# Performance work log

Measured on AMD Instinct MI355X. Metric: run time of the kernel, lower is better.

Reference implementation:

```python
import jax, jax.numpy as jnp
import numpy as np

N_NODES = 50000
N_EDGES = 800000
D_IN = 128
D_HID = 128
D_OUT = 128


def _glorot(key, shape):
    fan_in, fan_out = shape
    lim = np.sqrt(6.0 / (fan_in + fan_out))
    return jax.random.uniform(key, shape, jnp.float32, -lim, lim)


def setup_inputs() -> dict:
    key = jax.random.key(0)
    ks = jax.random.split(key, 8)
    x = jax.random.normal(ks[0], (N_NODES, D_IN), jnp.float32)
    edge_index = jax.random.randint(ks[1], (2, N_EDGES), 0, N_NODES, jnp.int64)
    # SAGEConv layer 1: lin_l (neighbor aggregate, has bias), lin_r (root, no bias)
    W1l = _glorot(ks[2], (D_IN, D_HID))
    b1 = jnp.zeros((D_HID,), jnp.float32)
    W1r = _glorot(ks[3], (D_IN, D_HID))
    # SAGEConv layer 2
    W2l = _glorot(ks[4], (D_HID, D_OUT))
    b2 = jnp.zeros((D_OUT,), jnp.float32)
    W2r = _glorot(ks[5], (D_HID, D_OUT))
    return {"x": x, "edge_index": edge_index, "W1l": W1l, "b1": b1,
            "W1r": W1r, "W2l": W2l, "b2": b2, "W2r": W2r}


def _sage_conv(x, src, dst, Wl, bl, Wr):
    # mean-aggregate neighbor features j -> i, then out = mean @ Wl + b + x @ Wr
    msg_sum = jax.ops.segment_sum(x[src], dst, num_segments=N_NODES)  # [N, F]
    cnt = jax.ops.segment_sum(jnp.ones((src.shape[0],), x.dtype), dst,
                              num_segments=N_NODES)  # [N]
    mean = msg_sum / jnp.maximum(cnt, 1.0)[:, None]
    return mean @ Wl + bl + x @ Wr


def reference(x, edge_index, W1l, b1, W1r, W2l, b2, W2r):
    src, dst = edge_index[0], edge_index[1]
    h = _sage_conv(x, src, dst, W1l, b1, W1r)
    h = jax.nn.relu(h)
    # dropout(p=0.2) is identity in eval mode
    out = _sage_conv(h, src, dst, W2l, b2, W2r)
    return out
```

## Files before the change

### kernel.cpp

```cpp
#include <hip/hip_runtime.h>

#define N_NODES 50000
#define N_EDGES 800000
#define D 128
#define CAP 64
#define NPB 512
#define NBIN 98
#define BIN_CAP 12288
#define EPB 4096

typedef __attribute__((ext_vector_type(8))) short s16x8;
typedef __attribute__((ext_vector_type(8))) unsigned short u16x8;
typedef __attribute__((ext_vector_type(4))) unsigned short u16x4;
typedef __attribute__((ext_vector_type(4))) float f32x4;

__device__ __forceinline__ unsigned short f2bf(float f) {
    unsigned u = __builtin_bit_cast(unsigned, f);
    return (unsigned short)((u + 0x7FFFu + ((u >> 16) & 1u)) >> 16);
}
__device__ __forceinline__ float bf2f(unsigned short h) {
    return __builtin_bit_cast(float, (unsigned)h << 16);
}

__device__ __forceinline__ int load_src(const int* ei, int is32, int e) {
    return is32 ? ei[e] : ei[2 * e];
}
__device__ __forceinline__ int load_dst(const int* ei, int is32, int e) {
    return is32 ? ei[N_EDGES + e] : ei[2 * N_EDGES + 2 * e];
}

__global__ void zbin_kernel(int* __restrict__ bin_cnt) {
    bin_cnt[threadIdx.x] = 0;
}

__global__ __launch_bounds__(256) void prepbin_kernel(
    const float* __restrict__ x, const int* __restrict__ ei,
    const float* __restrict__ W1l, const float* __restrict__ W1r,
    const float* __restrict__ W2l, const float* __restrict__ W2r,
    unsigned short* __restrict__ xb, unsigned short* __restrict__ wt1,
    unsigned short* __restrict__ wt2, int* __restrict__ bin_cnt,
    unsigned* __restrict__ bins) {
    __shared__ unsigned sBuf[EPB];
    __shared__ int bcnt[128], brun[128], bpos[128], gbase[128];
    __shared__ int sAny;
    int b = blockIdx.x;
    int tid = threadIdx.x;
    if (b < 3125) {
        int t = b * 256 + tid;
        float4 a = *(const float4*)(x + (size_t)t * 8);
        float4 c = *(const float4*)(x + (size_t)t * 8 + 4);
        u16x8 o;
        o[0] = f2bf(a.x); o[1] = f2bf(a.y); o[2] = f2bf(a.z); o[3] = f2bf(a.w);
        o[4] = f2bf(c.x); o[5] = f2bf(c.y); o[6] = f2bf(c.z); o[7] = f2bf(c.w);
        *(u16x8*)(xb + (size_t)t * 8) = o;
        return;
    }
    if (b < 3381) {
        int idx = b - 3125;
        int layer = idx >> 7;
        int c = idx & 127;
        const float* Wl = layer ? W2l : W1l;
        const float* Wr = layer ? W2r : W1r;
        unsigned short* wt = layer ? wt2 : wt1;
        float v = (tid < 128) ? Wl[(size_t)tid * 128 + c]
                              : Wr[(size_t)(tid - 128) * 128 + c];
        wt[c * 256 + tid] = f2bf(v);
        return;
    }
    int blk = b - 3381;
    int e0 = blk * EPB + tid * 16;
    int nblk = N_EDGES - blk * EPB;
    if (nblk > EPB) nblk = EPB;
    bool valid = (tid * 16) < nblk;
    if (tid == 0) sAny = 0;
    if (tid < 128) bcnt[tid] = 0;
    __syncthreads();
    if (ei[2 * tid + 1] != 0) atomicOr(&sAny, 1);
    __syncthreads();
    int is32 = sAny;
    unsigned packed[16];
    if (valid) {
        if (is32) {
            const int4* ps = (const int4*)(ei + e0);
            const int4* pd = (const int4*)(ei + N_EDGES + e0);
#pragma unroll
            for (int q = 0; q < 4; ++q) {
                int4 s = ps[q], d = pd[q];
                packed[q * 4 + 0] = ((unsigned)d.x << 16) | (unsigned)s.x;
                packed[q * 4 + 1] = ((unsigned)d.y << 16) | (unsigned)s.y;
                packed[q * 4 + 2] = ((unsigned)d.z << 16) | (unsigned)s.z;
                packed[q * 4 + 3] = ((unsigned)d.w << 16) | (unsigned)s.w;
            }
        } else {
            const int4* ps = (const int4*)(ei + 2 * (size_t)e0);
            const int4* pd = (const int4*)(ei + 2 * (size_t)N_EDGES + 2 * (size_t)e0);
#pragma unroll
            for (int q = 0; q < 8; ++q) {
                int4 s = ps[q], d = pd[q];
                packed[q * 2 + 0] = ((unsigned)d.x << 16) | (unsigned)s.x;
                packed[q * 2 + 1] = ((unsigned)d.z << 16) | (unsigned)s.z;
            }
        }
#pragma unroll
        for (int k = 0; k < 16; ++k) atomicAdd(&bcnt[packed[k] >> 25], 1);
    }
    __syncthreads();
    if (tid < 64) {
        int a = bcnt[2 * tid], bb = bcnt[2 * tid + 1];
        int s = a + bb;
        int incl = s;
#pragma unroll
        for (int o = 1; o < 64; o <<= 1) {
            int t = __shfl_up(incl, o, 64);
            if (tid >= o) incl += t;
        }
        int pref = incl - s;
        brun[2 * tid] = pref;
        brun[2 * tid + 1] = pref + a;
        bpos[2 * tid] = pref;
        bpos[2 * tid + 1] = pref + a;
    }
    __syncthreads();
    if (valid) {
#pragma unroll
        for (int k = 0; k < 16; ++k) {
            int bin = packed[k] >> 25;
            int slot = atomicAdd(&bpos[bin], 1);
            sBuf[slot] = packed[k];
        }
    }
    __syncthreads();
    if (tid < 128) {
        int n = bcnt[tid];
        gbase[tid] = n > 0 ? atomicAdd(&bin_cnt[tid], n) : 0;
    }
    __syncthreads();
    for (int i = tid; i < nblk; i += 256) {
        unsigned p = sBuf[i];
        int bin = p >> 25;
        int gpos = gbase[bin] + (i - brun[bin]);
        if (gpos < BIN_CAP) bins[(size_t)bin * BIN_CAP + gpos] = p;
    }
}

__global__ __launch_bounds__(256) void unbin_kernel(const int* __restrict__ bin_cnt,
                                                    const unsigned* __restrict__ bins,
                                                    int* __restrict__ cnt,
                                                    unsigned short* __restrict__ srcs16) {
    __shared__ unsigned short buck[NPB * CAP];
    __shared__ int lcnt[NPB];
    int tid = threadIdx.x;
    int bn = blockIdx.x;
    int nbase = bn * NPB;
    for (int i = tid; i < NPB; i += 256) lcnt[i] = 0;
    __syncthreads();
    int nE = bin_cnt[bn];
    if (nE > BIN_CAP) nE = BIN_CAP;
    for (int i = tid; i < nE; i += 256) {
        unsigned p = bins[(size_t)bn * BIN_CAP + i];
        int local = (int)(p >> 16) - nbase;
        if ((unsigned)local < NPB) {
            int slot = atomicAdd(&lcnt[local], 1);
            if (slot < CAP) buck[local * CAP + slot] = (unsigned short)(p & 0xFFFFu);
        }
    }
    __syncthreads();
    int nlim = N_NODES - nbase;
    if (nlim > NPB) nlim = NPB;
    const uint4* sb = (const uint4*)buck;
    uint4* go = (uint4*)(srcs16 + (size_t)nbase * CAP);
    int n4 = nlim * 8;
    for (int i = tid; i < n4; i += 256) go[i] = sb[i];
    for (int i = tid; i < nlim; i += 256) cnt[nbase + i] = lcnt[i];
}

__global__ __launch_bounds__(256) void aggp_kernel(const unsigned short* __restrict__ feat,
                                                   const int* __restrict__ cnt,
                                                   const unsigned short* __restrict__ srcs16,
                                                   unsigned short* __restrict__ agg) {
    int node = blockIdx.x * 4 + (threadIdx.x >> 6);
    if (node >= N_NODES) return;
    int lane = threadIdx.x & 63;
    int q = lane >> 4;
    int c16 = lane & 15;
    int deg = cnt[node];
    int idx = srcs16[(size_t)node * CAP + lane];
    int d = deg < CAP ? deg : CAP;
    float acc[8] = {};
    for (int j = 0; j < d; j += 16) {
        int e[4];
        float m[4];
#pragma unroll
        for (int u = 0; u < 4; ++u) {
            int jj = j + u * 4 + q;
            int es = __shfl(idx, jj, 64);
            bool val = jj < d;
            e[u] = val ? es : 0;
            m[u] = val ? 1.f : 0.f;
        }
        u16x8 v[4];
#pragma unroll
        for (int u = 0; u < 4; ++u)
            v[u] = *((const u16x8*)(feat + (size_t)e[u] * D) + c16);
#pragma unroll
        for (int u = 0; u < 4; ++u)
#pragma unroll
            for (int i = 0; i < 8; ++i)
                acc[i] += bf2f((unsigned short)v[u][i]) * m[u];
    }
#pragma unroll
    for (int i = 0; i < 8; ++i) {
        acc[i] += __shfl_xor(acc[i], 16, 64);
        acc[i] += __shfl_xor(acc[i], 32, 64);
    }
    if (q == 0) {
        float s = deg > 0 ? 1.f / (float)deg : 0.f;
        u16x8 o;
#pragma unroll
        for (int i = 0; i < 8; ++i) o[i] = f2bf(acc[i] * s);
        *((u16x8*)(agg + (size_t)node * D) + c16) = o;
    }
}

template <int MODE>
__global__ __launch_bounds__(256) void mm3_kernel(const unsigned short* __restrict__ Agb,
                                                  const unsigned short* __restrict__ Rootb,
                                                  const unsigned short* __restrict__ Wt,
                                                  const float* __restrict__ bias,
                                                  float* __restrict__ C,
                                                  unsigned short* __restrict__ Cb) {
    __shared__ __align__(16) unsigned short sA[2][32][128];
    int r0 = blockIdx.x * 32;
    int tid = threadIdx.x;
    int lane = tid & 63, wid = tid >> 6;
    int l15 = lane & 15, khalf = lane >> 4;

    s16x8 bF[2][4][2];
#pragma unroll
    for (int p = 0; p < 2; ++p)
#pragma unroll
        for (int kc2 = 0; kc2 < 4; ++kc2)
#pragma unroll
            for (int nf = 0; nf < 2; ++nf) {
                int cc = wid * 32 + nf * 16 + l15;
                bF[p][kc2][nf] = *(const s16x8*)(Wt + (size_t)cc * 256 + p * 128 +
                                                 kc2 * 32 + khalf * 8);
            }
    {
        int r = tid >> 3;
        int kq = tid & 7;
        int row = r0 + r;
        u16x8 a0, a1, x0, x1;
        if (row < N_NODES) {
            const u16x8* pa = (const u16x8*)(Agb + (size_t)row * D + kq * 16);
            a0 = pa[0]; a1 = pa[1];
            const u16x8* pr = (const u16x8*)(Rootb + (size_t)row * D + kq * 16);
            x0 = pr[0]; x1 = pr[1];
        } else {
            u16x8 z = {};
            a0 = z; a1 = z; x0 = z; x1 = z;
        }
        int c0 = (kq * 2) ^ (r & 7), c1 = (kq * 2 + 1) ^ (r & 7);
        *(u16x8*)&sA[0][r][c0 * 8] = a0;
        *(u16x8*)&sA[0][r][c1 * 8] = a1;
        *(u16x8*)&sA[1][r][c0 * 8] = x0;
        *(u16x8*)&sA[1][r][c1 * 8] = x1;
    }
    __syncthreads();

    f32x4 acc[2][2] = {};
#pragma unroll
    for (int p = 0; p < 2; ++p)
#pragma unroll
        for (int kc2 = 0; kc2 < 4; ++kc2) {
            s16x8 aF[2];
#pragma unroll
            for (int mf = 0; mf < 2; ++mf) {
                int rr = mf * 16 + l15;
                int chunk = (kc2 * 4 + khalf) ^ (rr & 7);
                aF[mf] = *(const s16x8*)&sA[p][rr][chunk * 8];
            }
#pragma unroll
            for (int nf = 0; nf < 2; ++nf)
#pragma unroll
                for (int mf = 0; mf < 2; ++mf)
                    acc[mf][nf] = __builtin_amdgcn_mfma_f32_16x16x32_bf16(
                        aF[mf], bF[p][kc2][nf], acc[mf][nf], 0, 0, 0);
        }

#pragma unroll
    for (int mf = 0; mf < 2; ++mf)
#pragma unroll
        for (int nf = 0; nf < 2; ++nf) {
            int col = wid * 32 + nf * 16 + l15;
            float b = bias[col];
#pragma unroll
            for (int r = 0; r < 4; ++r) {
                int row = r0 + mf * 16 + khalf * 4 + r;
                if (row < N_NODES) {
                    float o = acc[mf][nf][r] + b;
                    if (MODE == 1) {
                        o = fmaxf(o, 0.f);
                        Cb[(size_t)row * D + col] = f2bf(o);
                    } else {
                        C[(size_t)row * D + col] = o;
                    }
                }
            }
        }
}

__global__ void initc_kernel(const int* __restrict__ ei, int* __restrict__ flag,
                             int* __restrict__ cnt) {
    int i = blockIdx.x * 256 + threadIdx.x;
    if (i < 50048) cnt[i] = 0;
    if (blockIdx.x == 0) {
        __shared__ int any;
        if (threadIdx.x == 0) any = 0;
        __syncthreads();
        if (ei[2 * threadIdx.x + 1] != 0) atomicOr(&any, 1);
        __syncthreads();
        if (threadIdx.x == 0) flag[0] = any;
    }
}

__global__ void prep_wf_kernel(const float* __restrict__ W1l, const float* __restrict__ W1r,
                               const float* __restrict__ W2l, const float* __restrict__ W2r,
                               unsigned short* __restrict__ wt1,
                               unsigned short* __restrict__ wt2) {
    int layer = blockIdx.x >> 7;
    int c = blockIdx.x & 127;
    int k = threadIdx.x;
    const float* Wl = layer ? W2l : W1l;
    const float* Wr = layer ? W2r : W1r;
    unsigned short* wt = layer ? wt2 : wt1;
    float v = (k < 128) ? Wl[(size_t)k * 128 + c] : Wr[(size_t)(k - 128) * 128 + c];
    wt[c * 256 + k] = f2bf(v);
}

__global__ void tobf_kernel(const float* __restrict__ in, unsigned short* __restrict__ out,
                            int n8) {
    int t = blockIdx.x * 256 + threadIdx.x;
    if (t >= n8) return;
    float4 a = *(const float4*)(in + (size_t)t * 8);
    float4 b = *(const float4*)(in + (size_t)t * 8 + 4);
    u16x8 o;
    o[0] = f2bf(a.x); o[1] = f2bf(a.y); o[2] = f2bf(a.z); o[3] = f2bf(a.w);
    o[4] = f2bf(b.x); o[5] = f2bf(b.y); o[6] = f2bf(b.z); o[7] = f2bf(b.w);
    *(u16x8*)(out + (size_t)t * 8) = o;
}

__global__ void hist_kernel(const int* __restrict__ ei, const int* __restrict__ flag,
                            int* __restrict__ cnt) {
    int e = blockIdx.x * blockDim.x + threadIdx.x;
    if (e >= N_EDGES) return;
    int is32 = flag[0];
    atomicAdd(&cnt[load_dst(ei, is32, e)], 1);
}

__global__ __launch_bounds__(1024) void scan_kernel(int* __restrict__ cnt_cur,
                                                    int* __restrict__ off) {
    __shared__ int wsum[16];
    __shared__ int woff[16];
    __shared__ int carry;
    __shared__ int tile_tot;
    int lane = threadIdx.x & 63;
    int wid = threadIdx.x >> 6;
    if (threadIdx.x == 0) carry = 0;
    __syncthreads();
    for (int base = 0; base < N_NODES; base += 1024) {
        int i = base + threadIdx.x;
        int v = (i < N_NODES) ? cnt_cur[i] : 0;
        int incl = v;
#pragma unroll
        for (int o = 1; o < 64; o <<= 1) {
            int t = __shfl_up(incl, o, 64);
            if (lane >= o) incl += t;
        }
        if (lane == 63) wsum[wid] = incl;
        __syncthreads();
        if (wid == 0 && lane < 16) {
            int t = wsum[lane];
            int inc2 = t;
#pragma unroll
            for (int o = 1; o < 16; o <<= 1) {
                int u = __shfl_up(inc2, o, 64);
                if (lane >= o) inc2 += u;
            }
            woff[lane] = inc2 - t;
            if (lane == 15) tile_tot = inc2;
        }
        __syncthreads();
        int c = carry;
        if (i < N_NODES) {
            int o = c + woff[wid] + (incl - v);
            off[i] = o;
            cnt_cur[i] = o;
        }
        __syncthreads();
        if (threadIdx.x == 0) carry = c + tile_tot;
        __syncthreads();
    }
    if (threadIdx.x == 0) off[N_NODES] = carry;
}

__global__ void fillc_kernel(const int* __restrict__ ei, const int* __restrict__ flag,
                             int* __restrict__ cur, int* __restrict__ srcs) {
    int e = blockIdx.x * blockDim.x + threadIdx.x;
    if (e >= N_EDGES) return;
    int is32 = flag[0];
    int d = load_dst(ei, is32, e);
    int p = atomicAdd(&cur[d], 1);
    srcs[p] = load_src(ei, is32, e);
}

__global__ __launch_bounds__(256) void aggc_kernel(const unsigned short* __restrict__ feat,
                                                   const int* __restrict__ off,
                                                   const int* __restrict__ srcs,
                                                   unsigned short* __restrict__ agg) {
    int node = blockIdx.x * 4 + (threadIdx.x >> 6);
    if (node >= N_NODES) return;
    int lane = threadIdx.x & 63;
    int half = lane >> 5;
    int c8 = lane & 31;
    int s0 = off[node], s1 = off[node + 1];
    int deg = s1 - s0;
    float a0 = 0.f, a1 = 0.f, a2 = 0.f, a3 = 0.f;
    for (int j = s0; j < s1; j += 2) {
        int jj = j + half;
        if (jj < s1) {
            int e = srcs[jj];
            u16x4 v = *((const u16x4*)(feat + (size_t)e * D) + c8);
            a0 += bf2f((unsigned short)v[0]);
            a1 += bf2f((unsigned short)v[1]);
            a2 += bf2f((unsigned short)v[2]);
            a3 += bf2f((unsigned short)v[3]);
        }
    }
    a0 += __shfl_xor(a0, 32, 64);
    a1 += __shfl_xor(a1, 32, 64);
    a2 += __shfl_xor(a2, 32, 64);
    a3 += __shfl_xor(a3, 32, 64);
    if (half == 0) {
        float s = deg > 0 ? 1.f / (float)deg : 0.f;
        u16x4 o;
        o[0] = f2bf(a0 * s); o[1] = f2bf(a1 * s);
        o[2] = f2bf(a2 * s); o[3] = f2bf(a3 * s);
        *((u16x4*)(agg + (size_t)node * D) + c8) = o;
    }
}

extern "C" void kernel_launch(void* const* d_in, const int* in_sizes, int n_in,
                              void* d_out, int out_size, void* d_ws, size_t ws_size,
                              hipStream_t stream) {
    const float* x = (const float*)d_in[0];
    const int* ei = (const int*)d_in[1];
    const float* W1l = (const float*)d_in[2];
    const float* b1 = (const float*)d_in[3];
    const float* W1r = (const float*)d_in[4];
    const float* W2l = (const float*)d_in[5];
    const float* b2 = (const float*)d_in[6];
    const float* W2r = (const float*)d_in[7];
    float* out = (float*)d_out;

    const size_t padded_need = 512 + (size_t)NBIN * BIN_CAP * 4 +
                               (size_t)50176 * CAP * 2 + 50048 * 4 + 2 * 65536 +
                               2 * (size_t)N_NODES * D * 2;

    if (ws_size >= padded_need) {
        char* w = (char*)d_ws;
        int* bin_cnt = (int*)w;                   w += 512;
        unsigned* bins = (unsigned*)w;            w += (size_t)NBIN * BIN_CAP * 4;
        unsigned short* srcs16 = (unsigned short*)w; w += (size_t)50176 * CAP * 2;
        int* cnt = (int*)w;                       w += 50048 * 4;
        unsigned short* wt1 = (unsigned short*)w; w += 65536;
        unsigned short* wt2 = (unsigned short*)w; w += 65536;
        unsigned short* xb = (unsigned short*)w;  w += (size_t)N_NODES * D * 2;
        unsigned short* hb = (unsigned short*)w;

        zbin_kernel<<<1, 128, 0, stream>>>(bin_cnt);
        prepbin_kernel<<<3577, 256, 0, stream>>>(x, ei, W1l, W1r, W2l, W2r, xb, wt1,
                                                 wt2, bin_cnt, bins);
        unbin_kernel<<<NBIN, 256, 0, stream>>>(bin_cnt, bins, cnt, srcs16);

        int nblk = (N_NODES + 31) / 32;
        aggp_kernel<<<(N_NODES + 3) / 4, 256, 0, stream>>>(xb, cnt, srcs16, hb);
        mm3_kernel<1><<<nblk, 256, 0, stream>>>(hb, xb, wt1, b1, nullptr, xb);

        aggp_kernel<<<(N_NODES + 3) / 4, 256, 0, stream>>>(xb, cnt, srcs16, hb);
        mm3_kernel<2><<<nblk, 256, 0, stream>>>(hb, xb, wt2, b2, out, nullptr);
    } else {
        char* w = (char*)d_ws;
        int* flag = (int*)w;                      w += 256;
        int* cur = (int*)w;                       w += 50048 * 4;
        int* off = (int*)w;                       w += 50056 * 4;
        int* srcs = (int*)w;                      w += (size_t)N_EDGES * 4;
        unsigned short* wt1 = (unsigned short*)w; w += 65536;
        unsigned short* wt2 = (unsigned short*)w; w += 65536;
        unsigned short* xb = (unsigned short*)w;  w += (size_t)N_NODES * D * 2;
        unsigned short* aggb = (unsigned short*)w;

        initc_kernel<<<196, 256, 0, stream>>>(ei, flag, cur);
        prep_wf_kernel<<<256, 256, 0, stream>>>(W1l, W1r, W2l, W2r, wt1, wt2);
        tobf_kernel<<<(N_NODES * D / 8 + 255) / 256, 256, 0, stream>>>(x, xb, N_NODES * D / 8);
        hist_kernel<<<(N_EDGES + 255) / 256, 256, 0, stream>>>(ei, flag, cur);
        scan_kernel<<<1, 1024, 0, stream>>>(cur, off);
        fillc_kernel<<<(N_EDGES + 255) / 256, 256, 0, stream>>>(ei, flag, cur, srcs);

        int nblk = (N_NODES + 31) / 32;
        aggc_kernel<<<(N_NODES + 3) / 4, 256, 0, stream>>>(xb, off, srcs, aggb);
        mm3_kernel<1><<<nblk, 256, 0, stream>>>(aggb, xb, wt1, b1, nullptr, xb);

        aggc_kernel<<<(N_NODES + 3) / 4, 256, 0, stream>>>(xb, off, srcs, aggb);
        mm3_kernel<2><<<nblk, 256, 0, stream>>>(aggb, xb, wt2, b2, out, nullptr);
    }
}
```

Baseline: 131.8 us.

## Fuse neighbor mean aggregation with dual-matmul into one kernel per layer

Replaces the separate aggregation and matmul kernels with a single 1024-thread kernel per layer. Each of 16 waves aggregates one node into shared memory, then the waves split the two K-halves (aggregate and root) across MFMA and reduce the partial results through shared memory. This removes the global round trip of the aggregated bf16 buffer and two launches per forward pass. In exchange it uses a small 16-row tile with reloaded weight fragments per block and an extra LDS reduction stage. The layer-1 output now goes to a separate buffer instead of overwriting xb.

```diff
diff --git a/kernel.cpp b/kernel.cpp
--- a/kernel.cpp
+++ b/kernel.cpp
@@ -174,140 +174,101 @@
     for (int i = tid; i < nlim; i += 256) cnt[nbase + i] = lcnt[i];
 }
 
-__global__ __launch_bounds__(256) void aggp_kernel(const unsigned short* __restrict__ feat,
-                                                   const int* __restrict__ cnt,
-                                                   const unsigned short* __restrict__ srcs16,
-                                                   unsigned short* __restrict__ agg) {
-    int node = blockIdx.x * 4 + (threadIdx.x >> 6);
-    if (node >= N_NODES) return;
-    int lane = threadIdx.x & 63;
-    int q = lane >> 4;
-    int c16 = lane & 15;
-    int deg = cnt[node];
-    int idx = srcs16[(size_t)node * CAP + lane];
-    int d = deg < CAP ? deg : CAP;
-    float acc[8] = {};
-    for (int j = 0; j < d; j += 16) {
-        int e[4];
-        float m[4];
-#pragma unroll
-        for (int u = 0; u < 4; ++u) {
-            int jj = j + u * 4 + q;
-            int es = __shfl(idx, jj, 64);
-            bool val = jj < d;
-            e[u] = val ? es : 0;
-            m[u] = val ? 1.f : 0.f;
-        }
-        u16x8 v[4];
-#pragma unroll
-        for (int u = 0; u < 4; ++u)
-            v[u] = *((const u16x8*)(feat + (size_t)e[u] * D) + c16);
-#pragma unroll
-        for (int u = 0; u < 4; ++u)
-#pragma unroll
-            for (int i = 0; i < 8; ++i)
-                acc[i] += bf2f((unsigned short)v[u][i]) * m[u];
-    }
-#pragma unroll
-    for (int i = 0; i < 8; ++i) {
-        acc[i] += __shfl_xor(acc[i], 16, 64);
-        acc[i] += __shfl_xor(acc[i], 32, 64);
-    }
-    if (q == 0) {
-        float s = deg > 0 ? 1.f / (float)deg : 0.f;
-        u16x8 o;
-#pragma unroll
-        for (int i = 0; i < 8; ++i) o[i] = f2bf(acc[i] * s);
-        *((u16x8*)(agg + (size_t)node * D) + c16) = o;
-    }
-}
-
 template <int MODE>
-__global__ __launch_bounds__(256) void mm3_kernel(const unsigned short* __restrict__ Agb,
-                                                  const unsigned short* __restrict__ Rootb,
-                                                  const unsigned short* __restrict__ Wt,
-                                                  const float* __restrict__ bias,
-                                                  float* __restrict__ C,
-                                                  unsigned short* __restrict__ Cb) {
-    __shared__ __align__(16) unsigned short sA[2][32][128];
-    int r0 = blockIdx.x * 32;
+__global__ __launch_bounds__(1024, 4) void fused16_kernel(
+    const unsigned short* __restrict__ feat,
+    const int* __restrict__ cnt,
+    const unsigned short* __restrict__ srcs16,
+    const unsigned short* __restrict__ Wt,
+    const float* __restrict__ bias,
+    float* __restrict__ C, unsigned short* __restrict__ Cb) {
+    __shared__ __align__(16) unsigned short sA[2][16][128];
+    __shared__ __align__(16) float sP[8][64][4];
+    int r0 = blockIdx.x * 16;
     int tid = threadIdx.x;
     int lane = tid & 63, wid = tid >> 6;
     int l15 = lane & 15, khalf = lane >> 4;
-
-    s16x8 bF[2][4][2];
-#pragma unroll
-    for (int p = 0; p < 2; ++p)
-#pragma unroll
-        for (int kc2 = 0; kc2 < 4; ++kc2)
-#pragma unroll
-            for (int nf = 0; nf < 2; ++nf) {
-                int cc = wid * 32 + nf * 16 + l15;
-                bF[p][kc2][nf] = *(const s16x8*)(Wt + (size_t)cc * 256 + p * 128 +
-                                                 kc2 * 32 + khalf * 8);
-            }
+    int p = wid >> 3, cf = wid & 7;
+
+    s16x8 bF[4];
+#pragma unroll
+    for (int kc2 = 0; kc2 < 4; ++kc2)
+        bF[kc2] = *(const s16x8*)(Wt + (size_t)(cf * 16 + l15) * 256 + p * 128 +
+                                  kc2 * 32 + khalf * 8);
+
+    if (tid < 256) {
+        int r = tid >> 4, ck = tid & 15;
+        u16x8 v = *(const u16x8*)(feat + (size_t)(r0 + r) * D + ck * 8);
+        *(u16x8*)&sA[1][r][(ck ^ (r & 7)) * 8] = v;
+    }
+
     {
-        int r = tid >> 3;
-        int kq = tid & 7;
-        int row = r0 + r;
-        u16x8 a0, a1, x0, x1;
-        if (row < N_NODES) {
-            const u16x8* pa = (const u16x8*)(Agb + (size_t)row * D + kq * 16);
-            a0 = pa[0]; a1 = pa[1];
-            const u16x8* pr = (const u16x8*)(Rootb + (size_t)row * D + kq * 16);
-            x0 = pr[0]; x1 = pr[1];
-        } else {
-            u16x8 z = {};
-            a0 = z; a1 = z; x0 = z; x1 = z;
-        }
-        int c0 = (kq * 2) ^ (r & 7), c1 = (kq * 2 + 1) ^ (r & 7);
-        *(u16x8*)&sA[0][r][c0 * 8] = a0;
-        *(u16x8*)&sA[0][r][c1 * 8] = a1;
-        *(u16x8*)&sA[1][r][c0 * 8] = x0;
-        *(u16x8*)&sA[1][r][c1 * 8] = x1;
-    }
-    __syncthreads();
-
-    f32x4 acc[2][2] = {};
-#pragma unroll
-    for (int p = 0; p < 2; ++p)
-#pragma unroll
-        for (int kc2 = 0; kc2 < 4; ++kc2) {
-            s16x8 aF[2];
-#pragma unroll
-            for (int mf = 0; mf < 2; ++mf) {
-                int rr = mf * 16 + l15;
-                int chunk = (kc2 * 4 + khalf) ^ (rr & 7);
-                aF[mf] = *(const s16x8*)&sA[p][rr][chunk * 8];
-            }
-#pragma unroll
-            for (int nf = 0; nf < 2; ++nf)
-#pragma unroll
-                for (int mf = 0; mf < 2; ++mf)
-                    acc[mf][nf] = __builtin_amdgcn_mfma_f32_16x16x32_bf16(
-                        aF[mf], bF[p][kc2][nf], acc[mf][nf], 0, 0, 0);
-        }
-
-#pragma unroll
-    for (int mf = 0; mf < 2; ++mf)
-#pragma unroll
-        for (int nf = 0; nf < 2; ++nf) {
-            int col = wid * 32 + nf * 16 + l15;
-            float b = bias[col];
-#pragma unroll
-            for (int r = 0; r < 4; ++r) {
-                int row = r0 + mf * 16 + khalf * 4 + r;
-                if (row < N_NODES) {
-                    float o = acc[mf][nf][r] + b;
-                    if (MODE == 1) {
-                        o = fmaxf(o, 0.f);
-                        Cb[(size_t)row * D + col] = f2bf(o);
-                    } else {
-                        C[(size_t)row * D + col] = o;
-                    }
-                }
-            }
-        }
+        int node = r0 + wid;
+        int deg = cnt[node];
+        int idx = srcs16[(size_t)node * CAP + lane];
+        int d = deg < CAP ? deg : CAP;
+        float acc[8] = {};
+        for (int j = 0; j < d; j += 16) {
+            int e[4];
+            float m[4];
+#pragma unroll
+            for (int u = 0; u < 4; ++u) {
+                int jj = j + u * 4 + khalf;
+                int es = __shfl(idx, jj, 64);
+                bool val = jj < d;
+                e[u] = val ? es : 0;
+                m[u] = val ? 1.f : 0.f;
+            }
+            u16x8 v[4];
+#pragma unroll
+            for (int u = 0; u < 4; ++u)
+                v[u] = *((const u16x8*)(feat + (size_t)e[u] * D) + l15);
+#pragma unroll
+            for (int u = 0; u < 4; ++u)
+#pragma unroll
+                for (int i = 0; i < 8; ++i)
+                    acc[i] += bf2f((unsigned short)v[u][i]) * m[u];
+        }
+#pragma unroll
+        for (int i = 0; i < 8; ++i) {
+            acc[i] += __shfl_xor(acc[i], 16, 64);
+            acc[i] += __shfl_xor(acc[i], 32, 64);
+        }
+        if (khalf == 0) {
+            float s = deg > 0 ? 1.f / (float)deg : 0.f;
+            u16x8 o;
+#pragma unroll
+            for (int i = 0; i < 8; ++i) o[i] = f2bf(acc[i] * s);
+            *(u16x8*)&sA[0][wid][(l15 ^ (wid & 7)) * 8] = o;
+        }
+    }
+    __syncthreads();
+
+    f32x4 acc2 = {};
+#pragma unroll
+    for (int kc2 = 0; kc2 < 4; ++kc2) {
+        int chunk = (kc2 * 4 + khalf) ^ (l15 & 7);
+        s16x8 aF = *(const s16x8*)&sA[p][l15][chunk * 8];
+        acc2 = __builtin_amdgcn_mfma_f32_16x16x32_bf16(aF, bF[kc2], acc2, 0, 0, 0);
+    }
+    if (p == 1) *(f32x4*)&sP[cf][lane][0] = acc2;
+    __syncthreads();
+    if (p == 0) {
+        f32x4 part = *(const f32x4*)&sP[cf][lane][0];
+        int col = cf * 16 + l15;
+        float b = bias[col];
+#pragma unroll
+        for (int r = 0; r < 4; ++r) {
+            int row = r0 + khalf * 4 + r;
+            float o = acc2[r] + part[r] + b;
+            if (MODE == 1) {
+                o = fmaxf(o, 0.f);
+                Cb[(size_t)row * D + col] = f2bf(o);
+            } else {
+                C[(size_t)row * D + col] = o;
+            }
+        }
+    }
 }
 
 __global__ void initc_kernel(const int* __restrict__ ei, int* __restrict__ flag,
@@ -450,6 +411,94 @@
     }
 }
 
+template <int MODE>
+__global__ __launch_bounds__(256) void mm3_kernel(const unsigned short* __restrict__ Agb,
+                                                  const unsigned short* __restrict__ Rootb,
+                                                  const unsigned short* __restrict__ Wt,
+                                                  const float* __restrict__ bias,
+                                                  float* __restrict__ C,
+                                                  unsigned short* __restrict__ Cb) {
+    __shared__ __align__(16) unsigned short sA[2][32][128];
+    int r0 = blockIdx.x * 32;
+    int tid = threadIdx.x;
+    int lane = tid & 63, wid = tid >> 6;
+    int l15 = lane & 15, khalf = lane >> 4;
+
+    s16x8 bF[2][4][2];
+#pragma unroll
+    for (int p = 0; p < 2; ++p)
+#pragma unroll
+        for (int kc2 = 0; kc2 < 4; ++kc2)
+#pragma unroll
+            for (int nf = 0; nf < 2; ++nf) {
+                int cc = wid * 32 + nf * 16 + l15;
+                bF[p][kc2][nf] = *(const s16x8*)(Wt + (size_t)cc * 256 + p * 128 +
+                                                 kc2 * 32 + khalf * 8);
+            }
+    {
+        int r = tid >> 3;
+        int kq = tid & 7;
+        int row = r0 + r;
+        u16x8 a0, a1, x0, x1;
+        if (row < N_NODES) {
+            const u16x8* pa = (const u16x8*)(Agb + (size_t)row * D + kq * 16);
+            a0 = pa[0]; a1 = pa[1];
+            const u16x8* pr = (const u16x8*)(Rootb + (size_t)row * D + kq * 16);
+            x0 = pr[0]; x1 = pr[1];
+        } else {
+            u16x8 z = {};
+            a0 = z; a1 = z; x0 = z; x1 = z;
+        }
+        int c0 = (kq * 2) ^ (r & 7), c1 = (kq * 2 + 1) ^ (r & 7);
+        *(u16x8*)&sA[0][r][c0 * 8] = a0;
+        *(u16x8*)&sA[0][r][c1 * 8] = a1;
+        *(u16x8*)&sA[1][r][c0 * 8] = x0;
+        *(u16x8*)&sA[1][r][c1 * 8] = x1;
+    }
+    __syncthreads();
+
+    f32x4 acc[2][2] = {};
+#pragma unroll
+    for (int p = 0; p < 2; ++p)
+#pragma unroll
+        for (int kc2 = 0; kc2 < 4; ++kc2) {
+            s16x8 aF[2];
+#pragma unroll
+            for (int mf = 0; mf < 2; ++mf) {
+                int rr = mf * 16 + l15;
+                int chunk = (kc2 * 4 + khalf) ^ (rr & 7);
+                aF[mf] = *(const s16x8*)&sA[p][rr][chunk * 8];
+            }
+#pragma unroll
+            for (int nf = 0; nf < 2; ++nf)
+#pragma unroll
+                for (int mf = 0; mf < 2; ++mf)
+                    acc[mf][nf] = __builtin_amdgcn_mfma_f32_16x16x32_bf16(
+                        aF[mf], bF[p][kc2][nf], acc[mf][nf], 0, 0, 0);
+        }
+
+#pragma unroll
+    for (int mf = 0; mf < 2; ++mf)
+#pragma unroll
+        for (int nf = 0; nf < 2; ++nf) {
+            int col = wid * 32 + nf * 16 + l15;
+            float b = bias[col];
+#pragma unroll
+            for (int r = 0; r < 4; ++r) {
+                int row = r0 + mf * 16 + khalf * 4 + r;
+                if (row < N_NODES) {
+                    float o = acc[mf][nf][r] + b;
+                    if (MODE == 1) {
+                        o = fmaxf(o, 0.f);
+                        Cb[(size_t)row * D + col] = f2bf(o);
+                    } else {
+                        C[(size_t)row * D + col] = o;
+                    }
+                }
+            }
+        }
+}
+
 extern "C" void kernel_launch(void* const* d_in, const int* in_sizes, int n_in,
                               void* d_out, int out_size, void* d_ws, size_t ws_size,
                               hipStream_t stream) {
@@ -483,12 +532,10 @@
                                                  wt2, bin_cnt, bins);
         unbin_kernel<<<NBIN, 256, 0, stream>>>(bin_cnt, bins, cnt, srcs16);
 
-        int nblk = (N_NODES + 31) / 32;
-        aggp_kernel<<<(N_NODES + 3) / 4, 256, 0, stream>>>(xb, cnt, srcs16, hb);
-        mm3_kernel<1><<<nblk, 256, 0, stream>>>(hb, xb, wt1, b1, nullptr, xb);
-
-        aggp_kernel<<<(N_NODES + 3) / 4, 256, 0, stream>>>(xb, cnt, srcs16, hb);
-        mm3_kernel<2><<<nblk, 256, 0, stream>>>(hb, xb, wt2, b2, out, nullptr);
+        fused16_kernel<1><<<3125, 1024, 0, stream>>>(xb, cnt, srcs16, wt1, b1,
+                                                     nullptr, hb);
+        fused16_kernel<2><<<3125, 1024, 0, stream>>>(hb, cnt, srcs16, wt2, b2,
+                                                     out, nullptr);
     } else {
         char* w = (char*)d_ws;
         int* flag = (int*)w;                      w += 256;
```

After: 165.9 us. 1.26x slower.
